# Kernel optimization log

Measured on AMD Instinct MI355X. Metric: run time of the kernel, lower is better.

Reference implementation:

```python
import jax, jax.numpy as jnp
import numpy as np

D_MODEL = 1024
N_HEAD = 16
HEAD_DIM = D_MODEL // N_HEAD  # 64


def setup_inputs() -> dict:
    key = jax.random.key(0)
    ks = jax.random.split(key, 8)
    B, T, C = 4, 2048, D_MODEL
    s = 0.02
    return {
        "q": jax.random.normal(ks[0], (B, T, C), jnp.float32),
        "k": jax.random.normal(ks[1], (B, T, C), jnp.float32),
        "v": jax.random.normal(ks[2], (B, T, C), jnp.float32),
        "Wq": jax.random.normal(ks[3], (C, C), jnp.float32) * s,
        "Wk": jax.random.normal(ks[4], (C, HEAD_DIM), jnp.float32) * s,
        "Wv": jax.random.normal(ks[5], (C, HEAD_DIM), jnp.float32) * s,
        "Wp": jax.random.normal(ks[6], (C, C), jnp.float32) * s,
        "bp": jnp.zeros((C,), jnp.float32),
    }


def reference(q, k, v, Wq, Wk, Wv, Wp, bp):
    B, T, C = q.shape
    scale = 1.0 / jnp.sqrt(jnp.asarray(HEAD_DIM, q.dtype))
    # projections (torch Linear: x @ W.T, here weights stored as [in, out])
    q_proj = (q @ Wq).reshape(B, T, N_HEAD, HEAD_DIM)  # [B,T,H,D]
    k_proj = k @ Wk  # [B,T,D] single shared KV head
    v_proj = v @ Wv  # [B,T,D]
    # full O(T^2) scores per head, shared K
    wei = jnp.einsum("bqhd,bkd->bhqk", q_proj, k_proj) * scale  # [B,H,T,T]
    p = jax.nn.softmax(wei, axis=-1)
    out = jnp.einsum("bhqk,bkd->bqhd", p, v_proj).reshape(B, T, C)
    return out @ Wp + bp  # dropout p=0.0 -> identity
```

## Files before the change

### kernel.cpp

```cpp
#include <hip/hip_runtime.h>
#include <hip/hip_bf16.h>


#define B_ 4
#define T_ 2048
#define C_ 1024
#define H_ 16
#define D_ 64
#define BT_ (B_*T_)
#define CS_ 0.1803368801111204f

typedef short bfrag __attribute__((ext_vector_type(8)));
typedef float f32x4 __attribute__((ext_vector_type(4)));

static __device__ inline short f2bf(float f){
    union { float f; unsigned u; } v; v.f = f;
    unsigned r = v.u + 0x7fffu + ((v.u >> 16) & 1u);
    return (short)(r >> 16);
}
#if __has_builtin(__builtin_amdgcn_cvt_pk_bf16_f32)
typedef __bf16 bf2_t __attribute__((ext_vector_type(2)));
static __device__ inline unsigned pk2(float a, float b){
    union { bf2_t v; unsigned u; } c;
    c.v = __builtin_amdgcn_cvt_pk_bf16_f32(a, b);
    return c.u;
}
#else
static __device__ inline unsigned pk2(float a, float b){
    return (unsigned)(unsigned short)f2bf(a) | ((unsigned)(unsigned short)f2bf(b) << 16);
}
#endif

#if __has_builtin(__builtin_amdgcn_global_load_lds)
#define HAVE_GLL 1
#define GLL16(g,l) __builtin_amdgcn_global_load_lds(                              \
    (const __attribute__((address_space(1))) void*)(g),                           \
    (__attribute__((address_space(3))) void*)(l), 16, 0, 0)
#else
#define HAVE_GLL 0
#define GLL16(g,l) (*(uint4*)(l) = *(const uint4*)(g))
#endif

#if __has_builtin(__builtin_amdgcn_exp2f)
#define EXP2(x) __builtin_amdgcn_exp2f(x)
#else
#define EXP2(x) __expf((x)*0.693147180559945f)
#endif

__global__ __launch_bounds__(256) void prep_kernel(
    const float* __restrict__ q,
    const float* __restrict__ Wq, const float* __restrict__ Wk,
    const float* __restrict__ Wv, const float* __restrict__ Wp,
    short* __restrict__ qb16,
    short* __restrict__ WqT, short* __restrict__ WkT,
    short* __restrict__ WvT, short* __restrict__ WpT)
{
    int bx = blockIdx.x, tid = threadIdx.x;
    if (bx < 4096) {
        int i = (bx * 256 + tid) * 8;
        float4 a = *(const float4*)(q + i);
        float4 b = *(const float4*)(q + i + 4);
        uint4 o; o.x = pk2(a.x,a.y); o.y = pk2(a.z,a.w);
                 o.z = pk2(b.x,b.y); o.w = pk2(b.z,b.w);
        *(uint4*)(qb16 + i) = o;
        return;
    }
    __shared__ short Ls[64][65];
    int b2 = bx - 4096;
    const float* W; short* Wt; int N, idx;
    if (b2 < 256)      { W = Wq; Wt = WqT; N = 1024; idx = b2; }
    else if (b2 < 272) { W = Wk; Wt = WkT; N = 64;   idx = b2 - 256; }
    else if (b2 < 288) { W = Wv; Wt = WvT; N = 64;   idx = b2 - 272; }
    else               { W = Wp; Wt = WpT; N = 1024; idx = b2 - 288; }
    int nx = N >> 6;
    int n0 = (idx % nx) * 64, k0 = (idx / nx) * 64;
    {
        int kr = tid >> 2, c4 = (tid & 3) * 16;
        const float* g = W + (size_t)(k0 + kr) * N + n0 + c4;
        #pragma unroll
        for (int e = 0; e < 16; e++) Ls[kr][c4 + e] = f2bf(g[e]);
    }
    __syncthreads();
    {
        int nr = tid >> 2, kc = (tid & 3) * 16;
        __align__(16) short tmp[16];
        #pragma unroll
        for (int e = 0; e < 16; e++) tmp[e] = Ls[kc + e][nr];
        short* o = Wt + (size_t)(n0 + nr) * 1024 + k0 + kc;
        *(uint4*)(o)     = *(uint4*)tmp;
        *(uint4*)(o + 8) = *(uint4*)(tmp + 8);
    }
}

__global__ __launch_bounds__(256) void kvproj_kernel(
    const float* __restrict__ Ksrc, const float* __restrict__ Vsrc,
    const short* __restrict__ WkT, const short* __restrict__ WvT,
    short* __restrict__ Kfo, short* __restrict__ Vfo)
{
    __shared__ __align__(16) short As[2048];
    __shared__ __align__(16) short Bs[2048];
    int mode = blockIdx.x >> 7;
    int m0 = (blockIdx.x & 127) * 64;
    const float* A  = mode ? Vsrc : Ksrc;
    const short* Bt = mode ? WvT : WkT;
    short* Out      = mode ? Vfo : Kfo;

    int tid = threadIdx.x, w = tid >> 6, lane = tid & 63;
    int quad = lane >> 4, l16 = lane & 15;
    int rowc = ((tid >> 6) << 4) + ((tid & 63) >> 2), oct = tid & 3;
    const float* ga = A + (size_t)(m0 + rowc) * C_ + oct * 8;
    const short* gb = Bt + (size_t)rowc * C_ + oct * 8;
    short* la = As + tid * 8; short* lb = Bs + tid * 8;

    f32x4 acc[4] = {};
    for (int k0 = 0; k0 < C_; k0 += 32) {
        __syncthreads();
        float4 fa = *(const float4*)(ga + k0);
        float4 fb = *(const float4*)(ga + k0 + 4);
        uint4 pa; pa.x = pk2(fa.x,fa.y); pa.y = pk2(fa.z,fa.w);
                  pa.z = pk2(fb.x,fb.y); pa.w = pk2(fb.z,fb.w);
        uint4 tb = *(const uint4*)(gb + k0);
        *(uint4*)la = pa; *(uint4*)lb = tb;
        __syncthreads();
        bfrag af = *(const bfrag*)(As + (w * 64 + l16 * 4 + quad) * 8);
        #pragma unroll
        for (int ni = 0; ni < 4; ni++) {
            bfrag bf = *(const bfrag*)(Bs + (ni * 64 + l16 * 4 + quad) * 8);
            acc[ni] = __builtin_amdgcn_mfma_f32_16x16x32_bf16(af, bf, acc[ni], 0, 0, 0);
        }
    }
    if (mode == 0) {
        #pragma unroll
        for (int ni = 0; ni < 4; ni++)
            #pragma unroll
            for (int r = 0; r < 4; r++) {
                int key = m0 + w * 16 + quad * 4 + r;
                int d = ni * 16 + l16;
                size_t adr = (size_t)(key >> 6) * 4096 +
                    ((((d >> 5) * 4 + ((key >> 4) & 3)) * 4 + ((d >> 3) & 3)) * 16 + (key & 15)) * 8 + (d & 7);
                Out[adr] = f2bf(acc[ni][r]);
            }
    } else {
        #pragma unroll
        for (int ni = 0; ni < 4; ni++) {
            int key = m0 + w * 16 + quad * 4;
            int tile = key >> 6, kfk = (key >> 5) & 1, qv = (key >> 3) & 3;
            int jb = (quad & 1) * 4;
            uint2 pk; pk.x = pk2(acc[ni][0], acc[ni][1]); pk.y = pk2(acc[ni][2], acc[ni][3]);
            *(uint2*)(Out + (size_t)tile * 4096 + (((kfk * 4 + ni) * 4 + qv) * 16 + l16) * 8 + jb) = pk;
        }
    }
}

__global__ __launch_bounds__(256) void attn_fused_kernel(
    const short* __restrict__ qb16, const short* __restrict__ WqT,
    const short* __restrict__ Kfo,  const short* __restrict__ Vfo,
    short* __restrict__ Out)
{
    __shared__ __align__(16) short lds[16384];
    int qb = blockIdx.x, h = blockIdx.y, b = blockIdx.z;
    int tid = threadIdx.x, w = tid >> 6, lane = tid & 63;
    int quad = lane >> 4, l16 = lane & 15;
    short* As = lds;
    short* Bs = lds + 4096;
    short* Ps = lds + w * 2048;
    short* Qs = lds + 8192 + w * 2048;

    {
        int m0q = b * T_ + qb * 128;
        int cA2 = tid + 256;
        int rA1 = ((tid >> 6) << 4) + ((tid & 63) >> 2), oA1 = tid & 3;
        int rA2 = ((cA2 >> 6) << 4) + ((cA2 & 63) >> 2), oA2 = cA2 & 3;
        const short* gA1 = qb16 + (size_t)(m0q + rA1) * C_ + oA1 * 8;
        const short* gA2 = qb16 + (size_t)(m0q + rA2) * C_ + oA2 * 8;
        const short* gB  = WqT + (size_t)(h * 64 + rA1) * C_ + oA1 * 8;
        short* lA1 = As + tid * 8; short* lA2 = As + cA2 * 8;
        short* lB  = Bs + tid * 8;

        f32x4 qacc[2][4] = {};
        for (int k0 = 0; k0 < C_; k0 += 32) {
            __syncthreads();
            GLL16(gA1 + k0, lA1); GLL16(gA2 + k0, lA2); GLL16(gB + k0, lB);
            __syncthreads();
            bfrag af[2], bf[4];
            #pragma unroll
            for (int mi = 0; mi < 2; mi++)
                af[mi] = *(const bfrag*)(As + ((w * 2 + mi) * 64 + l16 * 4 + quad) * 8);
            #pragma unroll
            for (int ni = 0; ni < 4; ni++)
                bf[ni] = *(const bfrag*)(Bs + (ni * 64 + l16 * 4 + quad) * 8);
            #pragma unroll
            for (int mi = 0; mi < 2; mi++)
                #pragma unroll
                for (int ni = 0; ni < 4; ni++)
                    qacc[mi][ni] = __builtin_amdgcn_mfma_f32_16x16x32_bf16(af[mi], bf[ni], qacc[mi][ni], 0, 0, 0);
        }
        #pragma unroll
        for (int mi = 0; mi < 2; mi++)
            #pragma unroll
            for (int ni = 0; ni < 4; ni++) {
                int base = ((ni >> 1) * 2 + mi) * 512 + ((ni & 1) * 2 + (l16 >> 3)) * 128 + (l16 & 7);
                #pragma unroll
                for (int r = 0; r < 4; r++)
                    Qs[base + (quad * 4 + r) * 8] = f2bf(qacc[mi][ni][r] * CS_);
            }
        __syncthreads();
    }

    bfrag qf[2][2];
    #pragma unroll
    for (int nb = 0; nb < 2; nb++)
        #pragma unroll
        for (int kf = 0; kf < 2; kf++)
            qf[nb][kf] = *(const bfrag*)(Qs + (kf * 2 + nb) * 512 + quad * 128 + l16 * 8);

    const short* Kb = Kfo + (size_t)b * (T_ * D_);
    const short* Vb = Vfo + (size_t)b * (T_ * D_);
    int q0 = qb * 128 + w * 32;

    f32x4 o[4][2] = {};
    float lsum[2] = {0.f, 0.f};
    int fragoff = (quad * 16 + l16) * 8;

    for (int t = 0; t < T_ / 64; t++) {
        const short* Kt = Kb + t * 4096;
        const short* Vt = Vb + t * 4096;
        bfrag ka[2][4];
        #pragma unroll
        for (int kf = 0; kf < 2; kf++)
            #pragma unroll
            for (int mi = 0; mi < 4; mi++)
                ka[kf][mi] = *(const bfrag*)(Kt + (kf * 4 + mi) * 512 + fragoff);
        f32x4 s[4][2];
        #pragma unroll
        for (int mi = 0; mi < 4; mi++)
            #pragma unroll
            for (int nb = 0; nb < 2; nb++) {
                f32x4 z = {};
                z = __builtin_amdgcn_mfma_f32_16x16x32_bf16(ka[0][mi], qf[nb][0], z, 0, 0, 0);
                z = __builtin_amdgcn_mfma_f32_16x16x32_bf16(ka[1][mi], qf[nb][1], z, 0, 0, 0);
                s[mi][nb] = z;
            }
        bfrag va[2][4];
        #pragma unroll
        for (int kf = 0; kf < 2; kf++)
            #pragma unroll
            for (int mi = 0; mi < 4; mi++)
                va[kf][mi] = *(const bfrag*)(Vt + (kf * 4 + mi) * 512 + fragoff);
        #pragma unroll
        for (int nb = 0; nb < 2; nb++) {
            #pragma unroll
            for (int mi = 0; mi < 4; mi++) {
                float p0 = EXP2(s[mi][nb][0]);
                float p1 = EXP2(s[mi][nb][1]);
                float p2 = EXP2(s[mi][nb][2]);
                float p3 = EXP2(s[mi][nb][3]);
                lsum[nb] += (p0 + p1) + (p2 + p3);
                uint2 pk; pk.x = pk2(p0, p1); pk.y = pk2(p2, p3);
                int kf = mi >> 1, qp_ = (mi & 1) * 2 + (quad >> 1), jb = (quad & 1) * 4;
                *(uint2*)(Ps + (kf * 2 + nb) * 512 + qp_ * 128 + l16 * 8 + jb) = pk;
            }
        }
        #pragma unroll
        for (int nb = 0; nb < 2; nb++) {
            bfrag pf0 = *(const bfrag*)(Ps + (0 + nb) * 512 + quad * 128 + l16 * 8);
            bfrag pf1 = *(const bfrag*)(Ps + (2 + nb) * 512 + quad * 128 + l16 * 8);
            #pragma unroll
            for (int mi = 0; mi < 4; mi++) {
                o[mi][nb] = __builtin_amdgcn_mfma_f32_16x16x32_bf16(va[0][mi], pf0, o[mi][nb], 0, 0, 0);
                o[mi][nb] = __builtin_amdgcn_mfma_f32_16x16x32_bf16(va[1][mi], pf1, o[mi][nb], 0, 0, 0);
            }
        }
    }
    #pragma unroll
    for (int nb = 0; nb < 2; nb++) {
        float l = lsum[nb];
        l += __shfl_xor(l, 16, 64);
        l += __shfl_xor(l, 32, 64);
        float rl = 1.0f / l;
        size_t row = (size_t)(b * T_ + q0 + nb * 16 + l16);
        #pragma unroll
        for (int mi = 0; mi < 4; mi++) {
            uint2 pk; pk.x = pk2(o[mi][nb][0] * rl, o[mi][nb][1] * rl);
                      pk.y = pk2(o[mi][nb][2] * rl, o[mi][nb][3] * rl);
            *(uint2*)(Out + row * C_ + h * 64 + mi * 16 + quad * 4) = pk;
        }
    }
}

__global__ __launch_bounds__(256) void gemm_fin_kernel(
    const short* __restrict__ A, const short* __restrict__ Bt,
    const float* __restrict__ bias, float* __restrict__ Out)
{
    __shared__ __align__(16) short As[8192];
    __shared__ __align__(16) short Bs[8192];
    const int N = C_, K = C_;
    int tid = threadIdx.x, w = tid >> 6, lane = tid & 63;
    int quad = lane >> 4, l16 = lane & 15;
    int wm = (w >> 1) * 64, wn = (w & 1) * 64;
    int m0 = blockIdx.y * 128, n0 = blockIdx.x * 128;

    const short* gA[4]; const short* gB[4]; short* lA[4]; short* lB[4];
    #pragma unroll
    for (int i = 0; i < 4; i++) {
        int c = tid + 256 * i;
        int row = ((c >> 7) << 4) + ((c & 63) >> 2);
        int koff = ((c >> 6) & 1) * 32 + (c & 3) * 8;
        gA[i] = A  + (size_t)(m0 + row) * K + koff;
        gB[i] = Bt + (size_t)(n0 + row) * K + koff;
        lA[i] = As + c * 8; lB[i] = Bs + c * 8;
    }

    f32x4 acc[4][4] = {};
    for (int k0 = 0; k0 < K; k0 += 64) {
        __syncthreads();
        #pragma unroll
        for (int i = 0; i < 4; i++) { GLL16(gA[i] + k0, lA[i]); GLL16(gB[i] + k0, lB[i]); }
        __syncthreads();
        #pragma unroll
        for (int ks = 0; ks < 2; ks++) {
            bfrag af[4], bf[4];
            #pragma unroll
            for (int i = 0; i < 4; i++) {
                af[i] = *(const bfrag*)(As + ((((wm >> 4) + i) * 2 + ks) * 64 + l16 * 4 + quad) * 8);
                bf[i] = *(const bfrag*)(Bs + ((((wn >> 4) + i) * 2 + ks) * 64 + l16 * 4 + quad) * 8);
            }
            #pragma unroll
            for (int mi = 0; mi < 4; mi++)
                #pragma unroll
                for (int ni = 0; ni < 4; ni++)
                    acc[mi][ni] = __builtin_amdgcn_mfma_f32_16x16x32_bf16(af[mi], bf[ni], acc[mi][ni], 0, 0, 0);
        }
    }
    #pragma unroll
    for (int mi = 0; mi < 4; mi++)
        #pragma unroll
        for (int ni = 0; ni < 4; ni++) {
            int col = n0 + wn + ni * 16 + l16;
            float bv = bias[col];
            #pragma unroll
            for (int r = 0; r < 4; r++) {
                int row = m0 + wm + mi * 16 + quad * 4 + r;
                Out[(size_t)row * N + col] = acc[mi][ni][r] + bv;
            }
        }
}

extern "C" void kernel_launch(void* const* d_in, const int* in_sizes, int n_in,
                              void* d_out, int out_size, void* d_ws, size_t ws_size,
                              hipStream_t stream) {
    const float* q  = (const float*)d_in[0];
    const float* k  = (const float*)d_in[1];
    const float* v  = (const float*)d_in[2];
    const float* Wq = (const float*)d_in[3];
    const float* Wk = (const float*)d_in[4];
    const float* Wv = (const float*)d_in[5];
    const float* Wp = (const float*)d_in[6];
    const float* bp = (const float*)d_in[7];
    float* out = (float*)d_out;

    char* ws = (char*)d_ws;
    short* qb16     = (short*)(ws);
    short* attn_out = (short*)(ws + (16u << 20));
    short* WqT  = (short*)(ws + (32u << 20));
    short* WpT  = (short*)(ws + (34u << 20));
    short* Kfo  = (short*)(ws + (36u << 20));
    short* Vfo  = (short*)(ws + (37u << 20));
    short* WkT  = (short*)(ws + (38u << 20));
    short* WvT  = (short*)(ws + (38u << 20) + (1u << 18));

    dim3 blk(256);
    prep_kernel<<<4640, blk, 0, stream>>>(q, Wq, Wk, Wv, Wp, qb16, WqT, WkT, WvT, WpT);
    kvproj_kernel<<<256, blk, 0, stream>>>(k, v, WkT, WvT, Kfo, Vfo);
    attn_fused_kernel<<<dim3(16, 16, 4), blk, 0, stream>>>(qb16, WqT, Kfo, Vfo, attn_out);
    gemm_fin_kernel<<<dim3(8, 64), blk, 0, stream>>>(attn_out, WpT, bp, out);
}
```

Baseline: 317.4 us.

## Shrink LDS and tiles across kernels to raise occupancy and block counts

The attention kernel drops its separate Q staging buffer and reuses the per-wave P region, halving its LDS so launch bounds can request four blocks per SM. The KV projection now uses 32-row tiles with a 64-wide k step, doubling the grid to 512 blocks. The final projection GEMM moves to 128x64 tiles, doubling its grid to 1024 blocks. These aim to fill more CUs and hide latency, at the cost of less data reuse per block and more register pressure from the occupancy hint.

```diff
diff --git a/kernel.cpp b/kernel.cpp
--- a/kernel.cpp
+++ b/kernel.cpp
@@ -32,12 +32,10 @@
 #endif
 
 #if __has_builtin(__builtin_amdgcn_global_load_lds)
-#define HAVE_GLL 1
 #define GLL16(g,l) __builtin_amdgcn_global_load_lds(                              \
     (const __attribute__((address_space(1))) void*)(g),                           \
     (__attribute__((address_space(3))) void*)(l), 16, 0, 0)
 #else
-#define HAVE_GLL 0
 #define GLL16(g,l) (*(uint4*)(l) = *(const uint4*)(g))
 #endif
 
@@ -98,73 +96,87 @@
     short* __restrict__ Kfo, short* __restrict__ Vfo)
 {
     __shared__ __align__(16) short As[2048];
-    __shared__ __align__(16) short Bs[2048];
-    int mode = blockIdx.x >> 7;
-    int m0 = (blockIdx.x & 127) * 64;
+    __shared__ __align__(16) short Bs[4096];
+    int mode = blockIdx.x >> 8;
+    int m0 = (blockIdx.x & 255) * 32;
     const float* A  = mode ? Vsrc : Ksrc;
     const short* Bt = mode ? WvT : WkT;
     short* Out      = mode ? Vfo : Kfo;
 
     int tid = threadIdx.x, w = tid >> 6, lane = tid & 63;
     int quad = lane >> 4, l16 = lane & 15;
-    int rowc = ((tid >> 6) << 4) + ((tid & 63) >> 2), oct = tid & 3;
-    const float* ga = A + (size_t)(m0 + rowc) * C_ + oct * 8;
-    const short* gb = Bt + (size_t)rowc * C_ + oct * 8;
-    short* la = As + tid * 8; short* lb = Bs + tid * 8;
-
-    f32x4 acc[4] = {};
-    for (int k0 = 0; k0 < C_; k0 += 32) {
+    int wrow = (w >> 1) * 16, wcol = (w & 1) * 32;
+
+    int arow = tid >> 3, acol = (tid & 7) * 8;
+    int akh = acol >> 5, aoct = (acol >> 3) & 3;
+    short* asl = As + ((((arow >> 4) * 2 + akh) * 64 + (arow & 15) * 4 + aoct) * 8);
+    const float* ag = A + (size_t)(m0 + arow) * C_ + acol;
+    int brow = tid >> 2, bcol = (tid & 3) * 16;
+    int bkh = bcol >> 5, boct = (bcol >> 3) & 3;
+    short* bsl = Bs + ((((brow >> 4) * 2 + bkh) * 64 + (brow & 15) * 4 + boct) * 8);
+    const short* bg = Bt + (size_t)brow * C_ + bcol;
+
+    f32x4 acc[2] = {};
+    for (int k0 = 0; k0 < C_; k0 += 64) {
         __syncthreads();
-        float4 fa = *(const float4*)(ga + k0);
-        float4 fb = *(const float4*)(ga + k0 + 4);
-        uint4 pa; pa.x = pk2(fa.x,fa.y); pa.y = pk2(fa.z,fa.w);
-                  pa.z = pk2(fb.x,fb.y); pa.w = pk2(fb.z,fb.w);
-        uint4 tb = *(const uint4*)(gb + k0);
-        *(uint4*)la = pa; *(uint4*)lb = tb;
+        {
+            float4 fa = *(const float4*)(ag + k0);
+            float4 fb = *(const float4*)(ag + k0 + 4);
+            uint4 pa; pa.x = pk2(fa.x,fa.y); pa.y = pk2(fa.z,fa.w);
+                      pa.z = pk2(fb.x,fb.y); pa.w = pk2(fb.z,fb.w);
+            *(uint4*)asl = pa;
+            uint4 t0 = *(const uint4*)(bg + k0);
+            uint4 t1 = *(const uint4*)(bg + k0 + 8);
+            *(uint4*)bsl = t0; *(uint4*)(bsl + 8) = t1;
+        }
         __syncthreads();
-        bfrag af = *(const bfrag*)(As + (w * 64 + l16 * 4 + quad) * 8);
-        #pragma unroll
-        for (int ni = 0; ni < 4; ni++) {
-            bfrag bf = *(const bfrag*)(Bs + (ni * 64 + l16 * 4 + quad) * 8);
-            acc[ni] = __builtin_amdgcn_mfma_f32_16x16x32_bf16(af, bf, acc[ni], 0, 0, 0);
+        #pragma unroll
+        for (int ks = 0; ks < 2; ks++) {
+            bfrag af = *(const bfrag*)(As + (((wrow >> 4) * 2 + ks) * 64 + l16 * 4 + quad) * 8);
+            #pragma unroll
+            for (int ni = 0; ni < 2; ni++) {
+                int n = wcol + ni * 16;
+                bfrag bf = *(const bfrag*)(Bs + (((n >> 4) * 2 + ks) * 64 + l16 * 4 + quad) * 8);
+                acc[ni] = __builtin_amdgcn_mfma_f32_16x16x32_bf16(af, bf, acc[ni], 0, 0, 0);
+            }
         }
     }
     if (mode == 0) {
         #pragma unroll
-        for (int ni = 0; ni < 4; ni++)
+        for (int ni = 0; ni < 2; ni++)
             #pragma unroll
             for (int r = 0; r < 4; r++) {
-                int key = m0 + w * 16 + quad * 4 + r;
-                int d = ni * 16 + l16;
+                int key = m0 + wrow + quad * 4 + r;
+                int d = wcol + ni * 16 + l16;
                 size_t adr = (size_t)(key >> 6) * 4096 +
                     ((((d >> 5) * 4 + ((key >> 4) & 3)) * 4 + ((d >> 3) & 3)) * 16 + (key & 15)) * 8 + (d & 7);
                 Out[adr] = f2bf(acc[ni][r]);
             }
     } else {
         #pragma unroll
-        for (int ni = 0; ni < 4; ni++) {
-            int key = m0 + w * 16 + quad * 4;
+        for (int ni = 0; ni < 2; ni++) {
+            int ni2 = (w & 1) * 2 + ni;
+            int key = m0 + wrow + quad * 4;
             int tile = key >> 6, kfk = (key >> 5) & 1, qv = (key >> 3) & 3;
             int jb = (quad & 1) * 4;
             uint2 pk; pk.x = pk2(acc[ni][0], acc[ni][1]); pk.y = pk2(acc[ni][2], acc[ni][3]);
-            *(uint2*)(Out + (size_t)tile * 4096 + (((kfk * 4 + ni) * 4 + qv) * 16 + l16) * 8 + jb) = pk;
-        }
-    }
-}
-
-__global__ __launch_bounds__(256) void attn_fused_kernel(
+            *(uint2*)(Out + (size_t)tile * 4096 + (((kfk * 4 + ni2) * 4 + qv) * 16 + l16) * 8 + jb) = pk;
+        }
+    }
+}
+
+__global__ __launch_bounds__(256, 4) void attn_fused_kernel(
     const short* __restrict__ qb16, const short* __restrict__ WqT,
     const short* __restrict__ Kfo,  const short* __restrict__ Vfo,
     short* __restrict__ Out)
 {
-    __shared__ __align__(16) short lds[16384];
+    __shared__ __align__(16) short lds[8192];
     int qb = blockIdx.x, h = blockIdx.y, b = blockIdx.z;
     int tid = threadIdx.x, w = tid >> 6, lane = tid & 63;
     int quad = lane >> 4, l16 = lane & 15;
     short* As = lds;
     short* Bs = lds + 4096;
     short* Ps = lds + w * 2048;
-    short* Qs = lds + 8192 + w * 2048;
 
     {
         int m0q = b * T_ + qb * 128;
@@ -195,6 +207,7 @@
                 for (int ni = 0; ni < 4; ni++)
                     qacc[mi][ni] = __builtin_amdgcn_mfma_f32_16x16x32_bf16(af[mi], bf[ni], qacc[mi][ni], 0, 0, 0);
         }
+        __syncthreads();
         #pragma unroll
         for (int mi = 0; mi < 2; mi++)
             #pragma unroll
@@ -202,9 +215,8 @@
                 int base = ((ni >> 1) * 2 + mi) * 512 + ((ni & 1) * 2 + (l16 >> 3)) * 128 + (l16 & 7);
                 #pragma unroll
                 for (int r = 0; r < 4; r++)
-                    Qs[base + (quad * 4 + r) * 8] = f2bf(qacc[mi][ni][r] * CS_);
-            }
-        __syncthreads();
+                    Ps[base + (quad * 4 + r) * 8] = f2bf(qacc[mi][ni][r] * CS_);
+            }
     }
 
     bfrag qf[2][2];
@@ -212,7 +224,7 @@
     for (int nb = 0; nb < 2; nb++)
         #pragma unroll
         for (int kf = 0; kf < 2; kf++)
-            qf[nb][kf] = *(const bfrag*)(Qs + (kf * 2 + nb) * 512 + quad * 128 + l16 * 8);
+            qf[nb][kf] = *(const bfrag*)(Ps + (kf * 2 + nb) * 512 + quad * 128 + l16 * 8);
 
     const short* Kb = Kfo + (size_t)b * (T_ * D_);
     const short* Vb = Vfo + (size_t)b * (T_ * D_);
@@ -293,49 +305,60 @@
     const float* __restrict__ bias, float* __restrict__ Out)
 {
     __shared__ __align__(16) short As[8192];
-    __shared__ __align__(16) short Bs[8192];
+    __shared__ __align__(16) short Bs[4096];
     const int N = C_, K = C_;
     int tid = threadIdx.x, w = tid >> 6, lane = tid & 63;
     int quad = lane >> 4, l16 = lane & 15;
-    int wm = (w >> 1) * 64, wn = (w & 1) * 64;
-    int m0 = blockIdx.y * 128, n0 = blockIdx.x * 128;
-
-    const short* gA[4]; const short* gB[4]; short* lA[4]; short* lB[4];
+    int wm = (w >> 1) * 64, wn = (w & 1) * 32;
+    int m0 = blockIdx.y * 128, n0 = blockIdx.x * 64;
+
+    const short* gA[4]; short* lA[4];
     #pragma unroll
     for (int i = 0; i < 4; i++) {
         int c = tid + 256 * i;
         int row = ((c >> 7) << 4) + ((c & 63) >> 2);
         int koff = ((c >> 6) & 1) * 32 + (c & 3) * 8;
-        gA[i] = A  + (size_t)(m0 + row) * K + koff;
+        gA[i] = A + (size_t)(m0 + row) * K + koff;
+        lA[i] = As + c * 8;
+    }
+    const short* gB[2]; short* lB[2];
+    #pragma unroll
+    for (int i = 0; i < 2; i++) {
+        int c = tid + 256 * i;
+        int row = ((c >> 7) << 4) + ((c & 63) >> 2);
+        int koff = ((c >> 6) & 1) * 32 + (c & 3) * 8;
         gB[i] = Bt + (size_t)(n0 + row) * K + koff;
-        lA[i] = As + c * 8; lB[i] = Bs + c * 8;
-    }
-
-    f32x4 acc[4][4] = {};
+        lB[i] = Bs + c * 8;
+    }
+
+    f32x4 acc[4][2] = {};
     for (int k0 = 0; k0 < K; k0 += 64) {
         __syncthreads();
         #pragma unroll
-        for (int i = 0; i < 4; i++) { GLL16(gA[i] + k0, lA[i]); GLL16(gB[i] + k0, lB[i]); }
+        for (int i = 0; i < 4; i++) GLL16(gA[i] + k0, lA[i]);
+        #pragma unroll
+        for (int i = 0; i < 2; i++) GLL16(gB[i] + k0, lB[i]);
         __syncthreads();
         #pragma unroll
         for (int ks = 0; ks < 2; ks++) {
-            bfrag af[4], bf[4];
-            #pragma unroll
-            for (int i = 0; i < 4; i++) {
+            bfrag af[4], bf[2];
+            #pragma unroll
+            for (int i = 0; i < 4; i++)
                 af[i] = *(const bfrag*)(As + ((((wm >> 4) + i) * 2 + ks) * 64 + l16 * 4 + quad) * 8);
+            #pragma unroll
+            for (int i = 0; i < 2; i++)
                 bf[i] = *(const bfrag*)(Bs + ((((wn >> 4) + i) * 2 + ks) * 64 + l16 * 4 + quad) * 8);
-            }
             #pragma unroll
             for (int mi = 0; mi < 4; mi++)
                 #pragma unroll
-                for (int ni = 0; ni < 4; ni++)
+                for (int ni = 0; ni < 2; ni++)
                     acc[mi][ni] = __builtin_amdgcn_mfma_f32_16x16x32_bf16(af[mi], bf[ni], acc[mi][ni], 0, 0, 0);
         }
     }
     #pragma unroll
     for (int mi = 0; mi < 4; mi++)
         #pragma unroll
-        for (int ni = 0; ni < 4; ni++) {
+        for (int ni = 0; ni < 2; ni++) {
             int col = n0 + wn + ni * 16 + l16;
             float bv = bias[col];
             #pragma unroll
@@ -371,7 +394,7 @@
 
     dim3 blk(256);
     prep_kernel<<<4640, blk, 0, stream>>>(q, Wq, Wk, Wv, Wp, qb16, WqT, WkT, WvT, WpT);
-    kvproj_kernel<<<256, blk, 0, stream>>>(k, v, WkT, WvT, Kfo, Vfo);
+    kvproj_kernel<<<512, blk, 0, stream>>>(k, v, WkT, WvT, Kfo, Vfo);
     attn_fused_kernel<<<dim3(16, 16, 4), blk, 0, stream>>>(qb16, WqT, Kfo, Vfo, attn_out);
-    gemm_fin_kernel<<<dim3(8, 64), blk, 0, stream>>>(attn_out, WpT, bp, out);
-}
+    gemm_fin_kernel<<<dim3(16, 64), blk, 0, stream>>>(attn_out, WpT, bp, out);
+}
```

New measurement: 308.6 us. 2.8% less time.
